# Kernel optimization log

Measured on AMD Instinct MI355X. Metric: run time of the kernel, lower is better.

## Reference

```python
import jax, jax.numpy as jnp
from jax import lax
import numpy as np


def _pava_pool_idx(y):
    """Pool index per position for the non-decreasing PAVA isotonic fit of 1-D y.
    Stack-based pool-adjacent-violators: sums/cnts hold active pools, top is stack size.
    Returns int pool index (length n) mapping each position to its final pool."""
    n = y.shape[0]

    def step(carry, yi):
        su, ct, top = carry
        su = su.at[top].set(yi)
        ct = ct.at[top].set(1.0)
        top = top + 1

        def cond(s):
            s_, c_, t_ = s
            # violation: mean(pool[t-1]) < mean(pool[t-2]); cross-multiplied (cnts > 0).
            # safe when t_ == 1: index -1 holds zeros -> 0 < 0 is False.
            viol = s_[t_ - 1] * c_[t_ - 2] < s_[t_ - 2] * c_[t_ - 1]
            return (t_ >= 2) & viol

        def body(s):
            s_, c_, t_ = s
            s_ = s_.at[t_ - 2].add(s_[t_ - 1])
            c_ = c_.at[t_ - 2].add(c_[t_ - 1])
            return s_, c_, t_ - 1

        carry = lax.while_loop(cond, body, (su, ct, top))
        return carry, None

    init = (jnp.zeros(n, y.dtype), jnp.zeros(n, y.dtype), jnp.int32(0))
    (su, ct, top), _ = lax.scan(step, init, y)
    # pool j covers positions [ends[j-1], ends[j]); unused pools have ct == 0.
    ends = jnp.cumsum(ct)
    idx = jnp.searchsorted(ends, jnp.arange(n, dtype=ct.dtype), side='right')
    return idx


def _isotonic_nonincreasing_clip0(y):
    """sklearn isotonic_regression(y, y_min=0, increasing=False).
    Pools of the non-increasing fit of y == pools of the non-decreasing fit of -y.
    Final fitted value on each pool is the pool mean of y, clipped at 0."""
    n = y.shape[0]
    idx = _pava_pool_idx(-y)
    sums = jax.ops.segment_sum(y, idx, num_segments=n)
    cnts = jax.ops.segment_sum(jnp.ones_like(y), idx, num_segments=n)
    means = sums / jnp.maximum(cnts, 1.0)
    return jnp.maximum(means[idx], 0.0)


def _prox_owl(beta, weights):
    n = beta.shape[0]
    abs_b = jnp.abs(beta)
    order = jnp.argsort(-abs_b)               # descending |beta|
    iso_in = abs_b[order] - weights
    fit = _isotonic_nonincreasing_clip0(iso_in)
    # inverse permutation: idxs[ix] = arange(n)
    inv = jnp.zeros(n, jnp.int32).at[order].set(jnp.arange(n, dtype=jnp.int32))
    return jnp.sign(beta) * fit[inv]


def reference(u, x, weights):
    diff = (u - x).reshape(-1)
    proxd = _prox_owl(diff, weights)
    return x + proxd.reshape(x.shape)


def setup_inputs() -> dict:
    key = jax.random.key(0)
    k1, k2, k3 = jax.random.split(key, 3)
    shape = (1, 3, 224, 224)
    n = int(np.prod(shape))
    u = jax.random.normal(k1, shape, dtype=jnp.float32)
    x = jax.random.normal(k2, shape, dtype=jnp.float32)
    # OWL weights must be nonincreasing and nonnegative
    w = jnp.sort(jax.random.uniform(k3, (n,), dtype=jnp.float32))[::-1] * 0.01
    return {"u": u, "x": x, "weights": w}
```

## Files before the change

kernel.cpp:

```cpp
#include <hip/hip_runtime.h>
#include <stdint.h>
#include <math.h>

typedef unsigned long long u64;

#define NB 8192
#define BCAP 64
#define NSEG 8192
#define PBLK 64
#define NBLK (NSEG / PBLK)
#define MAXLC 24

__device__ __forceinline__ void merge_pair(
    int sL, int sR,
    int* shR, int* stRk, float* shS, float* shC, float* stS, float* stC,
    float* __restrict__ pSum, float* __restrict__ pCnt,
    int* __restrict__ prv, int* __restrict__ nxt) {
  int rR = shR[sR];
  if (rR < 0) return;
  if (shR[sL] < 0) {
    shR[sL] = rR; shS[sL] = shS[sR]; shC[sL] = shC[sR];
    stRk[sL] = stRk[sR]; stS[sL] = stS[sR]; stC[sL] = stC[sR];
    return;
  }
  int lR = stRk[sL];
  float lS = stS[sL], lC = stC[sL];
  float rS = shS[sR], rC = shC[sR];
  nxt[lR] = rR; prv[rR] = lR;
  if (rS * lC > lS * rC) {
    float MS = lS + rS, MC = lC + rC;
    int Mr = lR;
    bool rtail = (rR == stRk[sR]);
    pCnt[rR] = 0.f;
    int nx = nxt[rR];
    nxt[Mr] = nx; if (nx >= 0) prv[nx] = Mr;
    for (;;) {
      int pp = prv[Mr];
      if (pp >= 0) {
        float ps = pSum[pp], pc = pCnt[pp];
        if (MS * pc > ps * MC) {
          MS += ps; MC += pc;
          pCnt[Mr] = 0.f;
          int mn = nxt[Mr];
          nxt[pp] = mn; if (mn >= 0) prv[mn] = pp;
          Mr = pp;
          continue;
        }
      }
      int qq = nxt[Mr];
      if (qq >= 0) {
        float qs = pSum[qq], qc = pCnt[qq];
        if (qs * MC > MS * qc) {
          MS += qs; MC += qc;
          pCnt[qq] = 0.f;
          if (qq == stRk[sR]) rtail = true;
          int qn = nxt[qq];
          nxt[Mr] = qn; if (qn >= 0) prv[qn] = Mr;
          continue;
        }
      }
      break;
    }
    pSum[Mr] = MS; pCnt[Mr] = MC;
    if (Mr == shR[sL]) { shS[sL] = MS; shC[sL] = MC; }
    if (rtail) { stRk[sL] = Mr; stS[sL] = MS; stC[sL] = MC; }
    else       { stRk[sL] = stRk[sR]; stS[sL] = stS[sR]; stC[sL] = stC[sR]; }
  } else {
    stRk[sL] = stRk[sR]; stS[sL] = stS[sR]; stC[sL] = stC[sR];
  }
}

__device__ __forceinline__ void wave_bsort(const u64* src, u64* dst,
                                           int start, int cnt, int lane) {
  if (cnt == 1) {
    if (lane == 0) dst[start] = src[0];
    return;
  }
  if (cnt <= 64) {
    int W = 2;
    while (W < cnt) W <<= 1;
    u64 v0 = (lane < cnt) ? src[lane] : 0ull;
    for (int k = 2; k <= W; k <<= 1) {
      for (int j = k >> 1; j >= 1; j >>= 1) {
        bool up = ((lane & j) == 0);
        bool desc = ((lane & k) == 0);
        u64 p = __shfl_xor(v0, j);
        u64 mx = (v0 > p) ? v0 : p, mn = (v0 > p) ? p : v0;
        v0 = (up == desc) ? mx : mn;
      }
    }
    if (lane < cnt) dst[start + lane] = v0;
  } else {
    u64 v0 = (lane < cnt) ? src[lane] : 0ull;
    u64 v1 = (lane + 64 < cnt) ? src[lane + 64] : 0ull;
    for (int k = 2; k <= 128; k <<= 1) {
      for (int j = k >> 1; j >= 1; j >>= 1) {
        if (j == 64) {
          u64 mx = (v0 > v1) ? v0 : v1;
          u64 mn = (v0 > v1) ? v1 : v0;
          v0 = mx; v1 = mn;
        } else {
          bool up = ((lane & j) == 0);
          bool desc0 = ((lane & k) == 0);
          bool desc1 = (((lane + 64) & k) == 0);
          u64 p0 = __shfl_xor(v0, j);
          u64 p1 = __shfl_xor(v1, j);
          u64 mx0 = (v0 > p0) ? v0 : p0, mn0 = (v0 > p0) ? p0 : v0;
          v0 = (up == desc0) ? mx0 : mn0;
          u64 mx1 = (v1 > p1) ? v1 : p1, mn1 = (v1 > p1) ? p1 : v1;
          v1 = (up == desc1) ? mx1 : mn1;
        }
      }
    }
    if (lane < cnt) dst[start + lane] = v0;
    if (lane + 64 < cnt) dst[start + lane + 64] = v1;
  }
}

__global__ void k_init(const float* __restrict__ u, const float* __restrict__ x,
                       u64* __restrict__ keyPad, int* __restrict__ cursor, int n) {
  int i = blockIdx.x * blockDim.x + threadIdx.x;
  if (i >= n) return;
  float d = u[i] - x[i];
  float ad = fabsf(d);
  unsigned code = (d > 0.f) ? 2u : ((d < 0.f) ? 0u : 1u);
  u64 key = ((u64)__float_as_uint(ad) << 32) |
            (unsigned)(~(((unsigned)i << 2) | code));
  double v = erf(0.5 * (double)ad);
  int b = (int)(v * (double)NB);
  b = min(max(b, 0), NB - 1);
  int pos = atomicAdd(&cursor[b], 1);
  if (pos < BCAP) keyPad[(size_t)b * BCAP + pos] = key;
}

__global__ void __launch_bounds__(256) k_bsort(const u64* __restrict__ keyPad,
                                               u64* __restrict__ keyB,
                                               const int* __restrict__ cursor) {
  __shared__ int red[256];
  __shared__ int offs[4];
  int t = threadIdx.x;
  int b0 = blockIdx.x * 4;
  int sum = 0;
  for (int b = b0 + 4 + t; b < NB; b += 256) sum += min(cursor[b], BCAP);
  red[t] = sum;
  __syncthreads();
  for (int d = 128; d > 0; d >>= 1) {
    if (t < d) red[t] += red[t + d];
    __syncthreads();
  }
  if (t == 0) {
    int S = red[0];
    int c3 = min(cursor[b0 + 3], BCAP);
    int c2 = min(cursor[b0 + 2], BCAP);
    int c1 = min(cursor[b0 + 1], BCAP);
    offs[3] = S;
    offs[2] = S + c3;
    offs[1] = S + c3 + c2;
    offs[0] = S + c3 + c2 + c1;
  }
  __syncthreads();
  int wv = t >> 6, lane = t & 63;
  int b = b0 + wv;
  int cnt = min(cursor[b], BCAP);
  if (cnt == 0) return;
  wave_bsort(keyPad + (size_t)b * BCAP, keyB, offs[wv], cnt, lane);
}

__global__ void __launch_bounds__(64) k_pava_seg(
    const u64* __restrict__ key, const float* __restrict__ w,
    float* __restrict__ pSum, float* __restrict__ pCnt,
    int* __restrict__ prv, int* __restrict__ nxt,
    int* __restrict__ headR2, int* __restrict__ tailR2,
    float* __restrict__ headS2, float* __restrict__ headC2,
    float* __restrict__ tailS2, float* __restrict__ tailC2,
    int n, int Lc, int stride) {
  __shared__ float yv[PBLK * MAXLC], sS[PBLK * MAXLC], sC[PBLK * MAXLC];
  __shared__ int bHR[PBLK], bTR[PBLK];
  __shared__ float bHS[PBLK], bHC[PBLK], bTS[PBLK], bTC[PBLK];
  int t = threadIdx.x;
  int blk = blockIdx.x;
  int B0 = blk * PBLK * Lc;
  const unsigned* kh = (const unsigned*)key;
  int tot = PBLK * Lc;
  for (int i = t; i < tot; i += PBLK) {
    int g = B0 + i;
    float v = 0.f;
    if (g < n) v = __uint_as_float(kh[2 * g + 1]) - w[g];
    yv[(i / Lc) * stride + (i % Lc)] = v;
  }
  __syncthreads();
  int s = B0 + t * Lc;
  int e = min(s + Lc, n);
  if (s >= e) {
    bHR[t] = -1; bTR[t] = -1;
  } else {
    int cnt = e - s;
    int lb = t * stride;
    float ts = 0.f, tc = 0.f, ss = 0.f, sc = 0.f;
    int depth = 0;
    for (int r = 0; r < cnt; ++r) {
      float v = yv[lb + r];
      if (r > 0) {
        if (depth >= 1) { sS[lb + depth - 1] = ss; sC[lb + depth - 1] = sc; }
        ss = ts; sc = tc; ++depth;
      }
      ts = v; tc = 1.f;
      while (depth >= 1 && ts * sc > ss * tc) {
        ts += ss; tc += sc; --depth;
        if (depth >= 1) { ss = sS[lb + depth - 1]; sc = sC[lb + depth - 1]; }
      }
    }
    int prevStart = -1;
    int start = s;
    float hS = 0.f, hC = 0.f, lS = 0.f, lC = 0.f;
    for (int j = 0; j <= depth; ++j) {
      float sj, cj;
      if (j == depth)          { sj = ts; cj = tc; }
      else if (j == depth - 1) { sj = ss; cj = sc; }
      else                     { sj = sS[lb + j]; cj = sC[lb + j]; }
      if (j == 0) { hS = sj; hC = cj; }
      lS = sj; lC = cj;
      pSum[start] = sj; pCnt[start] = cj;
      prv[start] = prevStart;
      if (prevStart >= 0) nxt[prevStart] = start;
      int c = (int)cj;
      for (int z = 1; z < c; ++z) pCnt[start + z] = 0.f;
      prevStart = start;
      start += c;
    }
    nxt[prevStart] = -1;
    bHR[t] = s;  bTR[t] = prevStart;
    bHS[t] = hS; bHC[t] = hC;
    bTS[t] = lS; bTC[t] = lC;
  }
  __syncthreads();
  for (int step = 1; step < PBLK; step <<= 1) {
    int pairs = PBLK / (2 * step);
    if (t < pairs) {
      int sL = t * 2 * step;
      merge_pair(sL, sL + step, bHR, bTR, bHS, bHC, bTS, bTC, pSum, pCnt, prv, nxt);
    }
    __syncthreads();
  }
  if (t == 0) {
    headR2[blk] = bHR[0]; tailR2[blk] = bTR[0];
    headS2[blk] = bHS[0]; headC2[blk] = bHC[0];
    tailS2[blk] = bTS[0]; tailC2[blk] = bTC[0];
  }
}

__global__ void k_merge_pools(float* __restrict__ pSum, float* __restrict__ pCnt,
                              int* __restrict__ prv, int* __restrict__ nxt,
                              const int* __restrict__ headR, const int* __restrict__ tailR,
                              const float* __restrict__ headS, const float* __restrict__ headC,
                              const float* __restrict__ tailS, const float* __restrict__ tailC) {
  __shared__ int shR[NBLK], stRk[NBLK];
  __shared__ float shS[NBLK], shC[NBLK], stS[NBLK], stC[NBLK];
  int t = threadIdx.x;
  if (t < NBLK) {
    shR[t] = headR[t]; stRk[t] = tailR[t];
    shS[t] = headS[t]; shC[t] = headC[t];
    stS[t] = tailS[t]; stC[t] = tailC[t];
  }
  __syncthreads();
  for (int step = 1; step < NBLK; step <<= 1) {
    int pairs = NBLK / (2 * step);
    if (t < pairs) {
      int sL = t * 2 * step;
      merge_pair(sL, sL + step, shR, stRk, shS, shC, stS, stC, pSum, pCnt, prv, nxt);
    }
    __syncthreads();
  }
}

__global__ void k_scatter(const u64* __restrict__ key,
                          const float* __restrict__ pSum, const float* __restrict__ pCnt,
                          const float* __restrict__ x, float* __restrict__ out, int n) {
  int i = blockIdx.x * blockDim.x + threadIdx.x;
  if (i >= n) return;
  float c = pCnt[i];
  if (c > 0.f) {
    float m = fmaxf(pSum[i] / c, 0.f);
    int e = i + (int)c;
    for (int k = i; k < e; ++k) {
      unsigned r = ~(unsigned)(key[k] & 0xFFFFFFFFull);
      unsigned idx = r >> 2;
      unsigned code = r & 3u;
      float v = (code == 2u) ? m : ((code == 0u) ? -m : 0.f);
      out[idx] = x[idx] + v;
    }
  }
}

extern "C" void kernel_launch(void* const* d_in, const int* in_sizes, int n_in,
                              void* d_out, int out_size, void* d_ws, size_t ws_size,
                              hipStream_t stream) {
  const float* u = (const float*)d_in[0];
  const float* x = (const float*)d_in[1];
  const float* w = (const float*)d_in[2];
  float* out = (float*)d_out;
  int n = in_sizes[0];

  char* base = (char*)d_ws;
  u64* keyPad = (u64*)base;   base += (size_t)NB * BCAP * 8;
  u64* keyB   = (u64*)base;   base += (size_t)n * 8;
  float* pSum = (float*)base; base += (size_t)n * 4;
  float* pCnt = (float*)base; base += (size_t)n * 4;
  int* prv    = (int*)base;   base += (size_t)n * 4;
  int* nxt    = (int*)base;   base += (size_t)n * 4;
  int* cursor = (int*)base;   base += (size_t)NB * 4;
  int* headR2 = (int*)base;   base += NBLK * 4;
  int* tailR2 = (int*)base;   base += NBLK * 4;
  float* headS2 = (float*)base; base += NBLK * 4;
  float* headC2 = (float*)base; base += NBLK * 4;
  float* tailS2 = (float*)base; base += NBLK * 4;
  float* tailC2 = (float*)base; base += NBLK * 4;

  int gElem = (n + 255) / 256;
  int Lc = (n + NSEG - 1) / NSEG;
  int stride = (Lc & 1) ? Lc : Lc + 1;

  hipMemsetAsync(cursor, 0, (size_t)NB * 4, stream);
  hipLaunchKernelGGL(k_init, dim3(gElem), dim3(256), 0, stream,
                     u, x, keyPad, cursor, n);
  hipLaunchKernelGGL(k_bsort, dim3(NB / 4), dim3(256), 0, stream,
                     keyPad, keyB, cursor);
  hipLaunchKernelGGL(k_pava_seg, dim3(NBLK), dim3(PBLK), 0, stream,
                     keyB, w, pSum, pCnt, prv, nxt,
                     headR2, tailR2, headS2, headC2, tailS2, tailC2, n, Lc, stride);
  hipLaunchKernelGGL(k_merge_pools, dim3(1), dim3(NBLK), 0, stream,
                     pSum, pCnt, prv, nxt,
                     headR2, tailR2, headS2, headC2, tailS2, tailC2);
  hipLaunchKernelGGL(k_scatter, dim3(gElem), dim3(256), 0, stream,
                     keyB, pSum, pCnt, x, out, n);
}
```

Measured before the change: 103.6 us.

## Fuse per-bucket bitonic sort with local PAVA and merge buckets in-block

Merges the bucket sort kernel and the segment PAVA kernel into one kernel. Each wave sorts one bucket, computes y values directly from the sorted keys, and runs a serial PAVA on that bucket. Each block then merges its four bucket results before writing block head/tail summaries in reversed block order. The single-block final merge now spans 2048 segments with 1024 threads instead of 128. This removes one launch and a global round trip of keys, but it drops the 128-element path for buckets, so it assumes bucket counts never exceed 64 (BCAP). It also puts more tree levels into the serial single-block merge.

```diff
diff --git a/kernel.cpp b/kernel.cpp
--- a/kernel.cpp
+++ b/kernel.cpp
@@ -6,10 +6,7 @@
 
 #define NB 8192
 #define BCAP 64
-#define NSEG 8192
-#define PBLK 64
-#define NBLK (NSEG / PBLK)
-#define MAXLC 24
+#define NBLK2 (NB / 4)
 
 __device__ __forceinline__ void merge_pair(
     int sL, int sR,
@@ -70,53 +67,6 @@
   }
 }
 
-__device__ __forceinline__ void wave_bsort(const u64* src, u64* dst,
-                                           int start, int cnt, int lane) {
-  if (cnt == 1) {
-    if (lane == 0) dst[start] = src[0];
-    return;
-  }
-  if (cnt <= 64) {
-    int W = 2;
-    while (W < cnt) W <<= 1;
-    u64 v0 = (lane < cnt) ? src[lane] : 0ull;
-    for (int k = 2; k <= W; k <<= 1) {
-      for (int j = k >> 1; j >= 1; j >>= 1) {
-        bool up = ((lane & j) == 0);
-        bool desc = ((lane & k) == 0);
-        u64 p = __shfl_xor(v0, j);
-        u64 mx = (v0 > p) ? v0 : p, mn = (v0 > p) ? p : v0;
-        v0 = (up == desc) ? mx : mn;
-      }
-    }
-    if (lane < cnt) dst[start + lane] = v0;
-  } else {
-    u64 v0 = (lane < cnt) ? src[lane] : 0ull;
-    u64 v1 = (lane + 64 < cnt) ? src[lane + 64] : 0ull;
-    for (int k = 2; k <= 128; k <<= 1) {
-      for (int j = k >> 1; j >= 1; j >>= 1) {
-        if (j == 64) {
-          u64 mx = (v0 > v1) ? v0 : v1;
-          u64 mn = (v0 > v1) ? v1 : v0;
-          v0 = mx; v1 = mn;
-        } else {
-          bool up = ((lane & j) == 0);
-          bool desc0 = ((lane & k) == 0);
-          bool desc1 = (((lane + 64) & k) == 0);
-          u64 p0 = __shfl_xor(v0, j);
-          u64 p1 = __shfl_xor(v1, j);
-          u64 mx0 = (v0 > p0) ? v0 : p0, mn0 = (v0 > p0) ? p0 : v0;
-          v0 = (up == desc0) ? mx0 : mn0;
-          u64 mx1 = (v1 > p1) ? v1 : p1, mn1 = (v1 > p1) ? p1 : v1;
-          v1 = (up == desc1) ? mx1 : mn1;
-        }
-      }
-    }
-    if (lane < cnt) dst[start + lane] = v0;
-    if (lane + 64 < cnt) dst[start + lane + 64] = v1;
-  }
-}
-
 __global__ void k_init(const float* __restrict__ u, const float* __restrict__ x,
                        u64* __restrict__ keyPad, int* __restrict__ cursor, int n) {
   int i = blockIdx.x * blockDim.x + threadIdx.x;
@@ -133,11 +83,20 @@
   if (pos < BCAP) keyPad[(size_t)b * BCAP + pos] = key;
 }
 
-__global__ void __launch_bounds__(256) k_bsort(const u64* __restrict__ keyPad,
-                                               u64* __restrict__ keyB,
-                                               const int* __restrict__ cursor) {
+__global__ void __launch_bounds__(256) k_bsort_pava(
+    const u64* __restrict__ keyPad, u64* __restrict__ keyB,
+    const int* __restrict__ cursor, const float* __restrict__ w,
+    float* __restrict__ pSum, float* __restrict__ pCnt,
+    int* __restrict__ prv, int* __restrict__ nxt,
+    int* __restrict__ headR2, int* __restrict__ tailR2,
+    float* __restrict__ headS2, float* __restrict__ headC2,
+    float* __restrict__ tailS2, float* __restrict__ tailC2) {
   __shared__ int red[256];
-  __shared__ int offs[4];
+  __shared__ int offs4[4];
+  __shared__ float vals[4][BCAP], stS_[4][BCAP], stC_[4][BCAP];
+  __shared__ int qHR[4], qTR[4];
+  __shared__ float qHS[4], qHC[4], qTS[4], qTC[4];
+
   int t = threadIdx.x;
   int b0 = blockIdx.x * 4;
   int sum = 0;
@@ -153,120 +112,115 @@
     int c3 = min(cursor[b0 + 3], BCAP);
     int c2 = min(cursor[b0 + 2], BCAP);
     int c1 = min(cursor[b0 + 1], BCAP);
-    offs[3] = S;
-    offs[2] = S + c3;
-    offs[1] = S + c3 + c2;
-    offs[0] = S + c3 + c2 + c1;
-  }
-  __syncthreads();
+    offs4[3] = S;
+    offs4[2] = S + c3;
+    offs4[1] = S + c3 + c2;
+    offs4[0] = S + c3 + c2 + c1;
+  }
+  __syncthreads();
+
   int wv = t >> 6, lane = t & 63;
   int b = b0 + wv;
   int cnt = min(cursor[b], BCAP);
-  if (cnt == 0) return;
-  wave_bsort(keyPad + (size_t)b * BCAP, keyB, offs[wv], cnt, lane);
-}
-
-__global__ void __launch_bounds__(64) k_pava_seg(
-    const u64* __restrict__ key, const float* __restrict__ w,
+  int off = offs4[wv];
+  if (cnt > 0) {
+    const u64* src = keyPad + (size_t)b * BCAP;
+    u64 v0 = (lane < cnt) ? src[lane] : 0ull;
+    if (cnt > 1) {
+      int W = 2;
+      while (W < cnt) W <<= 1;
+      for (int k = 2; k <= W; k <<= 1) {
+        for (int j = k >> 1; j >= 1; j >>= 1) {
+          bool up = ((lane & j) == 0);
+          bool desc = ((lane & k) == 0);
+          u64 p = __shfl_xor(v0, j);
+          u64 mx = (v0 > p) ? v0 : p, mn = (v0 > p) ? p : v0;
+          v0 = (up == desc) ? mx : mn;
+        }
+      }
+    }
+    if (lane < cnt) {
+      keyB[off + lane] = v0;
+      vals[wv][lane] = __uint_as_float((unsigned)(v0 >> 32)) - w[off + lane];
+    }
+  }
+  __syncthreads();
+
+  if (lane == 0) {
+    int q = 3 - wv;
+    if (cnt == 0) {
+      qHR[q] = -1; qTR[q] = -1;
+    } else {
+      float ts = 0.f, tc = 0.f, ss = 0.f, sc = 0.f;
+      int depth = 0;
+      for (int r = 0; r < cnt; ++r) {
+        float v = vals[wv][r];
+        if (r > 0) {
+          if (depth >= 1) { stS_[wv][depth - 1] = ss; stC_[wv][depth - 1] = sc; }
+          ss = ts; sc = tc; ++depth;
+        }
+        ts = v; tc = 1.f;
+        while (depth >= 1 && ts * sc > ss * tc) {
+          ts += ss; tc += sc; --depth;
+          if (depth >= 1) { ss = stS_[wv][depth - 1]; sc = stC_[wv][depth - 1]; }
+        }
+      }
+      int prevStart = -1;
+      int start = off;
+      float hS = 0.f, hC = 0.f, lS = 0.f, lC = 0.f;
+      for (int j = 0; j <= depth; ++j) {
+        float sj, cj;
+        if (j == depth)          { sj = ts; cj = tc; }
+        else if (j == depth - 1) { sj = ss; cj = sc; }
+        else                     { sj = stS_[wv][j]; cj = stC_[wv][j]; }
+        if (j == 0) { hS = sj; hC = cj; }
+        lS = sj; lC = cj;
+        pSum[start] = sj; pCnt[start] = cj;
+        prv[start] = prevStart;
+        if (prevStart >= 0) nxt[prevStart] = start;
+        int c = (int)cj;
+        for (int z = 1; z < c; ++z) pCnt[start + z] = 0.f;
+        prevStart = start;
+        start += c;
+      }
+      nxt[prevStart] = -1;
+      qHR[q] = off;  qTR[q] = prevStart;
+      qHS[q] = hS; qHC[q] = hC;
+      qTS[q] = lS; qTC[q] = lC;
+    }
+  }
+  __syncthreads();
+  if (t == 0) merge_pair(0, 1, qHR, qTR, qHS, qHC, qTS, qTC, pSum, pCnt, prv, nxt);
+  if (t == 1) merge_pair(2, 3, qHR, qTR, qHS, qHC, qTS, qTC, pSum, pCnt, prv, nxt);
+  __syncthreads();
+  if (t == 0) {
+    merge_pair(0, 2, qHR, qTR, qHS, qHC, qTS, qTC, pSum, pCnt, prv, nxt);
+    int rb = NBLK2 - 1 - blockIdx.x;
+    headR2[rb] = qHR[0]; tailR2[rb] = qTR[0];
+    headS2[rb] = qHS[0]; headC2[rb] = qHC[0];
+    tailS2[rb] = qTS[0]; tailC2[rb] = qTC[0];
+  }
+}
+
+__global__ void __launch_bounds__(1024) k_merge_pools(
     float* __restrict__ pSum, float* __restrict__ pCnt,
     int* __restrict__ prv, int* __restrict__ nxt,
-    int* __restrict__ headR2, int* __restrict__ tailR2,
-    float* __restrict__ headS2, float* __restrict__ headC2,
-    float* __restrict__ tailS2, float* __restrict__ tailC2,
-    int n, int Lc, int stride) {
-  __shared__ float yv[PBLK * MAXLC], sS[PBLK * MAXLC], sC[PBLK * MAXLC];
-  __shared__ int bHR[PBLK], bTR[PBLK];
-  __shared__ float bHS[PBLK], bHC[PBLK], bTS[PBLK], bTC[PBLK];
+    const int* __restrict__ headR, const int* __restrict__ tailR,
+    const float* __restrict__ headS, const float* __restrict__ headC,
+    const float* __restrict__ tailS, const float* __restrict__ tailC) {
+  __shared__ int shR[NBLK2], stRk[NBLK2];
+  __shared__ float shS[NBLK2], shC[NBLK2], stS[NBLK2], stC[NBLK2];
   int t = threadIdx.x;
-  int blk = blockIdx.x;
-  int B0 = blk * PBLK * Lc;
-  const unsigned* kh = (const unsigned*)key;
-  int tot = PBLK * Lc;
-  for (int i = t; i < tot; i += PBLK) {
-    int g = B0 + i;
-    float v = 0.f;
-    if (g < n) v = __uint_as_float(kh[2 * g + 1]) - w[g];
-    yv[(i / Lc) * stride + (i % Lc)] = v;
-  }
-  __syncthreads();
-  int s = B0 + t * Lc;
-  int e = min(s + Lc, n);
-  if (s >= e) {
-    bHR[t] = -1; bTR[t] = -1;
-  } else {
-    int cnt = e - s;
-    int lb = t * stride;
-    float ts = 0.f, tc = 0.f, ss = 0.f, sc = 0.f;
-    int depth = 0;
-    for (int r = 0; r < cnt; ++r) {
-      float v = yv[lb + r];
-      if (r > 0) {
-        if (depth >= 1) { sS[lb + depth - 1] = ss; sC[lb + depth - 1] = sc; }
-        ss = ts; sc = tc; ++depth;
-      }
-      ts = v; tc = 1.f;
-      while (depth >= 1 && ts * sc > ss * tc) {
-        ts += ss; tc += sc; --depth;
-        if (depth >= 1) { ss = sS[lb + depth - 1]; sc = sC[lb + depth - 1]; }
-      }
-    }
-    int prevStart = -1;
-    int start = s;
-    float hS = 0.f, hC = 0.f, lS = 0.f, lC = 0.f;
-    for (int j = 0; j <= depth; ++j) {
-      float sj, cj;
-      if (j == depth)          { sj = ts; cj = tc; }
-      else if (j == depth - 1) { sj = ss; cj = sc; }
-      else                     { sj = sS[lb + j]; cj = sC[lb + j]; }
-      if (j == 0) { hS = sj; hC = cj; }
-      lS = sj; lC = cj;
-      pSum[start] = sj; pCnt[start] = cj;
-      prv[start] = prevStart;
-      if (prevStart >= 0) nxt[prevStart] = start;
-      int c = (int)cj;
-      for (int z = 1; z < c; ++z) pCnt[start + z] = 0.f;
-      prevStart = start;
-      start += c;
-    }
-    nxt[prevStart] = -1;
-    bHR[t] = s;  bTR[t] = prevStart;
-    bHS[t] = hS; bHC[t] = hC;
-    bTS[t] = lS; bTC[t] = lC;
-  }
-  __syncthreads();
-  for (int step = 1; step < PBLK; step <<= 1) {
-    int pairs = PBLK / (2 * step);
-    if (t < pairs) {
-      int sL = t * 2 * step;
-      merge_pair(sL, sL + step, bHR, bTR, bHS, bHC, bTS, bTC, pSum, pCnt, prv, nxt);
-    }
-    __syncthreads();
-  }
-  if (t == 0) {
-    headR2[blk] = bHR[0]; tailR2[blk] = bTR[0];
-    headS2[blk] = bHS[0]; headC2[blk] = bHC[0];
-    tailS2[blk] = bTS[0]; tailC2[blk] = bTC[0];
-  }
-}
-
-__global__ void k_merge_pools(float* __restrict__ pSum, float* __restrict__ pCnt,
-                              int* __restrict__ prv, int* __restrict__ nxt,
-                              const int* __restrict__ headR, const int* __restrict__ tailR,
-                              const float* __restrict__ headS, const float* __restrict__ headC,
-                              const float* __restrict__ tailS, const float* __restrict__ tailC) {
-  __shared__ int shR[NBLK], stRk[NBLK];
-  __shared__ float shS[NBLK], shC[NBLK], stS[NBLK], stC[NBLK];
-  int t = threadIdx.x;
-  if (t < NBLK) {
-    shR[t] = headR[t]; stRk[t] = tailR[t];
-    shS[t] = headS[t]; shC[t] = headC[t];
-    stS[t] = tailS[t]; stC[t] = tailC[t];
-  }
-  __syncthreads();
-  for (int step = 1; step < NBLK; step <<= 1) {
-    int pairs = NBLK / (2 * step);
-    if (t < pairs) {
-      int sL = t * 2 * step;
+  for (int i = t; i < NBLK2; i += 1024) {
+    shR[i] = headR[i]; stRk[i] = tailR[i];
+    shS[i] = headS[i]; shC[i] = headC[i];
+    stS[i] = tailS[i]; stC[i] = tailC[i];
+  }
+  __syncthreads();
+  for (int step = 1; step < NBLK2; step <<= 1) {
+    int pairs = NBLK2 / (2 * step);
+    for (int p = t; p < pairs; p += 1024) {
+      int sL = p * 2 * step;
       merge_pair(sL, sL + step, shR, stRk, shS, shC, stS, stC, pSum, pCnt, prv, nxt);
     }
     __syncthreads();
@@ -309,26 +263,22 @@
   int* prv    = (int*)base;   base += (size_t)n * 4;
   int* nxt    = (int*)base;   base += (size_t)n * 4;
   int* cursor = (int*)base;   base += (size_t)NB * 4;
-  int* headR2 = (int*)base;   base += NBLK * 4;
-  int* tailR2 = (int*)base;   base += NBLK * 4;
-  float* headS2 = (float*)base; base += NBLK * 4;
-  float* headC2 = (float*)base; base += NBLK * 4;
-  float* tailS2 = (float*)base; base += NBLK * 4;
-  float* tailC2 = (float*)base; base += NBLK * 4;
+  int* headR2 = (int*)base;   base += NBLK2 * 4;
+  int* tailR2 = (int*)base;   base += NBLK2 * 4;
+  float* headS2 = (float*)base; base += NBLK2 * 4;
+  float* headC2 = (float*)base; base += NBLK2 * 4;
+  float* tailS2 = (float*)base; base += NBLK2 * 4;
+  float* tailC2 = (float*)base; base += NBLK2 * 4;
 
   int gElem = (n + 255) / 256;
-  int Lc = (n + NSEG - 1) / NSEG;
-  int stride = (Lc & 1) ? Lc : Lc + 1;
 
   hipMemsetAsync(cursor, 0, (size_t)NB * 4, stream);
   hipLaunchKernelGGL(k_init, dim3(gElem), dim3(256), 0, stream,
                      u, x, keyPad, cursor, n);
-  hipLaunchKernelGGL(k_bsort, dim3(NB / 4), dim3(256), 0, stream,
-                     keyPad, keyB, cursor);
-  hipLaunchKernelGGL(k_pava_seg, dim3(NBLK), dim3(PBLK), 0, stream,
-                     keyB, w, pSum, pCnt, prv, nxt,
-                     headR2, tailR2, headS2, headC2, tailS2, tailC2, n, Lc, stride);
-  hipLaunchKernelGGL(k_merge_pools, dim3(1), dim3(NBLK), 0, stream,
+  hipLaunchKernelGGL(k_bsort_pava, dim3(NBLK2), dim3(256), 0, stream,
+                     keyPad, keyB, cursor, w, pSum, pCnt, prv, nxt,
+                     headR2, tailR2, headS2, headC2, tailS2, tailC2);
+  hipLaunchKernelGGL(k_merge_pools, dim3(1), dim3(1024), 0, stream,
                      pSum, pCnt, prv, nxt,
                      headR2, tailR2, headS2, headC2, tailS2, tailC2);
   hipLaunchKernelGGL(k_scatter, dim3(gElem), dim3(256), 0, stream,
```

After: 104.2 us. Within noise of the previous version (+0.6%).
